# Performance work log

Hardware: AMD Instinct MI355X
Metric: run time of the kernel (lower is better)

The kernel has to match this reference:

```python
import jax, jax.numpy as jnp
import numpy as np

B, NQ, NV = 4, 16384, 16384
DIM, FRAMES = 64, 4
D = DIM * FRAMES            # embed_dims = 256
HEADS, POINTS, LEVELS = 8, 4, 1
HD = D // HEADS             # head_dim = 32
HL, WL = 128, 128           # single-level feature map, HL*WL == NV
EPS = 1e-6


def setup_inputs() -> dict:
    key = jax.random.key(0)
    ks = jax.random.split(key, 14)
    inp = {
        "query": jax.random.normal(ks[0], (B, NQ, D), jnp.float32),
        "feat": jax.random.normal(ks[1], (B, NV, D), jnp.float32),
        "reference_points": jax.random.uniform(ks[2], (B, NQ, LEVELS, 2), jnp.float32),
        "spatial_shapes": jnp.array([[HL, WL]], jnp.int32),
        "level_start_index": jnp.array([0], jnp.int32),
        # LayerNorm params
        "qn_scale": jnp.ones((D,), jnp.float32),
        "qn_bias": jnp.zeros((D,), jnp.float32),
        "fn_scale": jnp.ones((D,), jnp.float32),
        "fn_bias": jnp.zeros((D,), jnp.float32),
        # MSDeformAttn projections
        "W_value": jax.random.normal(ks[3], (D, D), jnp.float32) / np.sqrt(D),
        "b_value": jnp.zeros((D,), jnp.float32),
        "W_off": jax.random.normal(ks[4], (D, HEADS * LEVELS * POINTS * 2), jnp.float32) * 0.01,
        "b_off": jax.random.normal(ks[5], (HEADS * LEVELS * POINTS * 2,), jnp.float32) * 0.5,
        "W_attn": jax.random.normal(ks[6], (D, HEADS * LEVELS * POINTS), jnp.float32) * 0.02,
        "b_attn": jnp.zeros((HEADS * LEVELS * POINTS,), jnp.float32),
        "W_out": jax.random.normal(ks[7], (D, D), jnp.float32) / np.sqrt(D),
        "b_out": jnp.zeros((D,), jnp.float32),
        # gamma is a learned scale (init 0 in the module; randomized here so it contributes)
        "gamma": jax.random.normal(ks[8], (D,), jnp.float32) * 0.1,
    }
    return inp


def _layer_norm(x, scale, bias):
    mu = jnp.mean(x, axis=-1, keepdims=True)
    var = jnp.mean(jnp.square(x - mu), axis=-1, keepdims=True)
    return (x - mu) * jax.lax.rsqrt(var + EPS) * scale + bias


def _bilinear_gather(v, loc, Hl, Wl):
    # v:   [B, H, N, hd] flattened level values (row-major HxW)
    # loc: [B, H, NQ, P, 2] normalized sampling locations in [0,1]
    # grid_sample semantics: align_corners=False, zero padding
    x = loc[..., 0] * Wl - 0.5
    y = loc[..., 1] * Hl - 0.5
    x0 = jnp.floor(x); y0 = jnp.floor(y)
    x1 = x0 + 1.0;     y1 = y0 + 1.0
    wx1 = x - x0; wx0 = 1.0 - wx1
    wy1 = y - y0; wy0 = 1.0 - wy1
    out = 0.0
    for xi, yi, w in ((x0, y0, wx0 * wy0), (x1, y0, wx1 * wy0),
                      (x0, y1, wx0 * wy1), (x1, y1, wx1 * wy1)):
        inb = (xi >= 0) & (xi < Wl) & (yi >= 0) & (yi < Hl)
        idx = (jnp.clip(yi, 0, Hl - 1) * Wl + jnp.clip(xi, 0, Wl - 1)).astype(jnp.int32)
        Bc, Hc, NQc, Pc = idx.shape
        g = jnp.take_along_axis(v, idx.reshape(Bc, Hc, NQc * Pc)[..., None], axis=2)
        g = g.reshape(Bc, Hc, NQc, Pc, -1)          # [B, H, NQ, P, hd]
        out = out + g * (w * inb)[..., None]
    return out


def reference(query, feat, reference_points, spatial_shapes, level_start_index,
              qn_scale, qn_bias, fn_scale, fn_bias,
              W_value, b_value, W_off, b_off, W_attn, b_attn, W_out, b_out, gamma):
    Bq, nq, _ = query.shape
    q = _layer_norm(query, qn_scale, qn_bias)
    v = _layer_norm(feat, fn_scale, fn_bias)

    # value projection -> per-head values [B, H, NV, hd]
    value = (v @ W_value + b_value).reshape(Bq, -1, HEADS, HD).transpose(0, 2, 1, 3)

    # sampling offsets [B, NQ, H, L, P, 2] and attention weights (softmax over L*P)
    off = (q @ W_off + b_off).reshape(Bq, nq, HEADS, LEVELS, POINTS, 2)
    aw = jax.nn.softmax((q @ W_attn + b_attn).reshape(Bq, nq, HEADS, LEVELS * POINTS), axis=-1)
    aw = aw.reshape(Bq, nq, HEADS, LEVELS, POINTS)

    ss = np.asarray(spatial_shapes)          # static level geometry
    lsi = np.asarray(level_start_index)
    offset_norm = ss[:, ::-1].astype(np.float32)  # (W, H) per level
    # sampling locations [B, NQ, H, L, P, 2]
    loc = reference_points[:, :, None, :, None, :] + off / offset_norm[None, None, None, :, None, :]

    acc = jnp.zeros((Bq, HEADS, nq, HD), query.dtype)
    for l in range(LEVELS):
        Hl, Wl = int(ss[l, 0]), int(ss[l, 1])
        start = int(lsi[l])
        v_l = value[:, :, start:start + Hl * Wl]                # [B, H, Hl*Wl, hd]
        loc_l = loc[:, :, :, l].transpose(0, 2, 1, 3, 4)        # [B, H, NQ, P, 2]
        sampled = _bilinear_gather(v_l, loc_l, Hl, Wl)          # [B, H, NQ, P, hd]
        aw_l = aw[:, :, :, l].transpose(0, 2, 1, 3)             # [B, H, NQ, P]
        acc = acc + jnp.einsum('bhnpd,bhnp->bhnd', sampled, aw_l)

    out = acc.transpose(0, 2, 1, 3).reshape(Bq, nq, D) @ W_out + b_out
    return query + gamma * out
```

## Files before the change

kernel.cpp:

```cpp
#include <hip/hip_runtime.h>

#define NQ 16384
#define NV 16384
#define DMODEL 256
#define SAMPN (4 * 16384 * 8)
#define VPLANE 65536

typedef __bf16 bf16x8 __attribute__((ext_vector_type(8)));
typedef float f32x4 __attribute__((ext_vector_type(4)));

__device__ __forceinline__ unsigned short f2bf(float x) {
    union { float f; unsigned int u; } v; v.f = x;
    unsigned int r = v.u + 0x7fff + ((v.u >> 16) & 1);
    return (unsigned short)(r >> 16);
}
__device__ __forceinline__ float blo(unsigned int u) {
    union { unsigned int u; float f; } v; v.u = u << 16; return v.f;
}
__device__ __forceinline__ float bhi(unsigned int u) {
    union { unsigned int u; float f; } v; v.u = u & 0xFFFF0000u; return v.f;
}
__device__ __forceinline__ f32x4 mfma16(bf16x8 a, bf16x8 b, f32x4 c) {
    return __builtin_amdgcn_mfma_f32_16x16x32_bf16(a, b, c, 0, 0, 0);
}

__global__ __launch_bounds__(256) void k_prep(
    const float* __restrict__ Wv, const float* __restrict__ Woff,
    const float* __restrict__ Wattn, const float* __restrict__ Wout,
    const float* __restrict__ fns, const float* __restrict__ fnb,
    const float* __restrict__ qns, const float* __restrict__ qnb,
    const float* __restrict__ b_value, const float* __restrict__ b_off,
    const float* __restrict__ b_attn,
    unsigned short* __restrict__ WtV, unsigned short* __restrict__ WtC,
    unsigned short* __restrict__ WtO,
    float* __restrict__ csumV, float* __restrict__ preV,
    float* __restrict__ csumC, float* __restrict__ preC) {
    const int blk = blockIdx.x;
    if (blk < 608) {
        int t = blk * 256 + threadIdx.x;
        if (t < 65536) { int n = t >> 8, k = t & 255; WtV[t] = f2bf(fns[k] * Wv[k * 256 + n]); return; }
        t -= 65536;
        if (t < 65536) { int n = t >> 8, k = t & 255; WtO[t] = f2bf(Wout[k * 256 + n]); return; }
        t -= 65536;
        if (t < 24576) {
            int j = t >> 8, k = t & 255;
            float w = (j < 64) ? Woff[k * 64 + j] : Wattn[k * 32 + (j - 64)];
            WtC[j * 256 + k] = f2bf(qns[k] * w);
        }
        return;
    }
    if (blk < 612) {
        __shared__ float sCS[4][64], sPR[4][64];
        const int nl = threadIdx.x & 63;
        const int n = (blk - 608) * 64 + nl;
        const int kp = threadIdx.x >> 6;
        float cs = 0.f, pr = 0.f;
        for (int k = kp * 64; k < kp * 64 + 64; ++k) {
            float w = Wv[k * 256 + n];
            cs += fns[k] * w;
            pr += fnb[k] * w;
        }
        sCS[kp][nl] = cs; sPR[kp][nl] = pr;
        __syncthreads();
        if (threadIdx.x < 64) {
            int nn = (blk - 608) * 64 + threadIdx.x;
            csumV[nn] = sCS[0][threadIdx.x] + sCS[1][threadIdx.x] + sCS[2][threadIdx.x] + sCS[3][threadIdx.x];
            preV[nn] = sPR[0][threadIdx.x] + sPR[1][threadIdx.x] + sPR[2][threadIdx.x] + sPR[3][threadIdx.x]
                       + b_value[nn];
        }
        return;
    }
    {
        __shared__ float sCS[2][96], sPR[2][96];
        const int t = threadIdx.x;
        if (t < 192) {
            const int n = t % 96;
            const int kp = t / 96;
            float cs = 0.f, pr = 0.f;
            for (int k = kp * 128; k < kp * 128 + 128; ++k) {
                float w = (n < 64) ? Woff[k * 64 + n] : Wattn[k * 32 + (n - 64)];
                cs += qns[k] * w;
                pr += qnb[k] * w;
            }
            sCS[kp][n] = cs; sPR[kp][n] = pr;
        }
        __syncthreads();
        if (t < 96) {
            csumC[t] = sCS[0][t] + sCS[1][t];
            preC[t] = sPR[0][t] + sPR[1][t] + ((t < 64) ? b_off[t] : b_attn[t - 64]);
        }
        return;
    }
}

__global__ __launch_bounds__(256) void k_hist(
    const float* __restrict__ refpt, int* __restrict__ hist) {
    const int q = blockIdx.x * 256 + threadIdx.x;
    const int b = q >> 14;
    float rx = refpt[(size_t)q * 2 + 0], ry = refpt[(size_t)q * 2 + 1];
    int px = min(max((int)(rx * 128.f), 0), 127);
    int py = min(max((int)(ry * 128.f), 0), 127);
    int bucket = (b << 8) | ((py >> 3) << 4) | (px >> 3);
    atomicAdd(&hist[bucket], 1);
}

__global__ __launch_bounds__(256) void k_scan(
    const int* __restrict__ hist, int* __restrict__ base, int* __restrict__ cursor) {
    __shared__ int tmp[256];
    const int t = threadIdx.x;
    int4 h4 = ((const int4*)hist)[t];
    int tsum = h4.x + h4.y + h4.z + h4.w;
    tmp[t] = tsum;
    __syncthreads();
    for (int d = 1; d < 256; d <<= 1) {
        int v = (t >= d) ? tmp[t - d] : 0;
        __syncthreads();
        tmp[t] += v;
        __syncthreads();
    }
    int excl = tmp[t] - tsum;
    int4 b4;
    b4.x = excl; b4.y = excl + h4.x; b4.z = b4.y + h4.y; b4.w = b4.z + h4.z;
    ((int4*)base)[t] = b4;
    ((int4*)cursor)[t] = b4;
}

__global__ __launch_bounds__(256) void k_perm(
    const float* __restrict__ refpt, int* __restrict__ cursor, int* __restrict__ perm) {
    const int q = blockIdx.x * 256 + threadIdx.x;
    const int b = q >> 14;
    float rx = refpt[(size_t)q * 2 + 0], ry = refpt[(size_t)q * 2 + 1];
    int px = min(max((int)(rx * 128.f), 0), 127);
    int py = min(max((int)(ry * 128.f), 0), 127);
    int bucket = (b << 8) | ((py >> 3) << 4) | (px >> 3);
    int slot = atomicAdd(&cursor[bucket], 1);
    perm[slot] = q;
}

#define STAGE_LNSTATS64(srcptr)                                                       \
    {                                                                                 \
        const int t = threadIdx.x;                                                    \
        const float4* src4 = (const float4*)((srcptr) + (size_t)m0 * 256);            \
        _Pragma("unroll 8") for (int i = 0; i < 16; ++i) {                            \
            float4 x = src4[i * 256 + t];                                             \
            const int row = i * 4 + (t >> 6);                                         \
            uint2 pk;                                                                 \
            pk.x = (unsigned)f2bf(x.x) | ((unsigned)f2bf(x.y) << 16);                 \
            pk.y = (unsigned)f2bf(x.z) | ((unsigned)f2bf(x.w) << 16);                 \
            *(uint2*)&A[row * 264 + (t & 63) * 4] = pk;                               \
        }                                                                             \
    }                                                                                 \
    __syncthreads();                                                                  \
    {                                                                                 \
        const int t = threadIdx.x;                                                    \
        const int r = t >> 2, h = t & 3;                                              \
        float s = 0.f, sq = 0.f;                                                      \
        _Pragma("unroll") for (int j = 0; j < 8; ++j) {                               \
            uint4 u = *(const uint4*)&A[r * 264 + h * 64 + j * 8];                    \
            float v0 = blo(u.x), v1 = bhi(u.x), v2 = blo(u.y), v3 = bhi(u.y);         \
            float v4 = blo(u.z), v5 = bhi(u.z), v6 = blo(u.w), v7 = bhi(u.w);         \
            s += v0 + v1 + v2 + v3 + v4 + v5 + v6 + v7;                               \
            sq += v0 * v0 + v1 * v1 + v2 * v2 + v3 * v3 +                             \
                  v4 * v4 + v5 * v5 + v6 * v6 + v7 * v7;                              \
        }                                                                             \
        s += __shfl_xor(s, 1);  sq += __shfl_xor(sq, 1);                              \
        s += __shfl_xor(s, 2);  sq += __shfl_xor(sq, 2);                              \
        if (h == 0) {                                                                 \
            float mu = s * 0.00390625f;                                               \
            muL[r] = mu;                                                              \
            rsL[r] = rsqrtf(sq * 0.00390625f - mu * mu + 1e-6f);                      \
        }                                                                             \
    }

#define MFMA_STEP4(bf, kk)                                                            \
    _Pragma("unroll") for (int m = 0; m < 4; ++m) {                                   \
        bf16x8 a = *(const bf16x8*)&A[(m * 16 + lrow) * 264 + (kk) * 32 + lk];        \
        _Pragma("unroll") for (int i = 0; i < 4; ++i)                                 \
            acc[i][m] = mfma16(bf[i], a, acc[i][m]);                                  \
    }

__global__ __launch_bounds__(256, 4) void k_mlp(
    const float* __restrict__ feat, const float* __restrict__ csumV,
    const float* __restrict__ preV, const unsigned short* __restrict__ WtV,
    unsigned short* __restrict__ value,
    const float* __restrict__ query, const float* __restrict__ refpt,
    const float* __restrict__ csumC, const float* __restrict__ preC,
    const unsigned short* __restrict__ WtC, float4* __restrict__ samples) {
    __shared__ unsigned short A[64 * 264];
    __shared__ float muL[64], rsL[64];
    const int blk = blockIdx.x;
    const int m0 = (blk >> 1) * 64;
    const int lane = threadIdx.x & 63;
    const int w = threadIdx.x >> 6;

    if ((blk & 1) == 0) {
        STAGE_LNSTATS64(feat)
        const int lrow = lane & 15, lk = (lane >> 4) * 8;
        f32x4 acc[4][4];
#pragma unroll
        for (int i = 0; i < 4; ++i)
#pragma unroll
            for (int m = 0; m < 4; ++m) acc[i][m] = (f32x4){0.f, 0.f, 0.f, 0.f};
#define LOADB_V(dst, kk)                                                              \
    _Pragma("unroll") for (int i = 0; i < 4; ++i) dst[i] =                            \
        *(const bf16x8*)(WtV + (size_t)((w * 4 + i) * 16 + lrow) * 256 + (kk) * 32 + lk);
        {
            bf16x8 b0[4], b1[4];
            LOADB_V(b0, 0)
#pragma unroll
            for (int k2 = 0; k2 < 4; ++k2) {
                LOADB_V(b1, k2 * 2 + 1)
                MFMA_STEP4(b0, k2 * 2)
                if (k2 < 3) { LOADB_V(b0, k2 * 2 + 2) }
                MFMA_STEP4(b1, k2 * 2 + 1)
            }
        }
        __syncthreads();
        const int g = lane >> 4;
#pragma unroll
        for (int i = 0; i < 4; ++i) {
            const int col0 = (w * 4 + i) * 16 + g * 4;
            float4 cs = *(const float4*)(csumV + col0);
            float4 pr = *(const float4*)(preV + col0);
#pragma unroll
            for (int m = 0; m < 4; ++m) {
                const int rl = m * 16 + (lane & 15);
                float mu = muL[rl], rs = rsL[rl];
                uint2 r;
                r.x = (unsigned)f2bf(rs * (acc[i][m][0] - mu * cs.x) + pr.x) |
                      ((unsigned)f2bf(rs * (acc[i][m][1] - mu * cs.y) + pr.y) << 16);
                r.y = (unsigned)f2bf(rs * (acc[i][m][2] - mu * cs.z) + pr.z) |
                      ((unsigned)f2bf(rs * (acc[i][m][3] - mu * cs.w) + pr.w) << 16);
                *(uint2*)&A[rl * 264 + col0] = r;
            }
        }
        __syncthreads();
        {
            const int pix = threadIdx.x >> 2;
            const int chunk = threadIdx.x & 3;
#pragma unroll
            for (int h = 0; h < 8; ++h) {
                *(uint4*)(value + ((size_t)h * VPLANE + (m0 + pix)) * 32 + chunk * 8) =
                    *(uint4*)&A[pix * 264 + h * 32 + chunk * 8];
            }
        }
    } else {
        float* DlA = (float*)A;
        const int lrow = lane & 15, g = lane >> 4, lk = g * 8;
        const float4* qrow = (const float4*)(query + (size_t)(m0 + w * 16 + lrow) * 256) + g * 2;
        f32x4 acc[6];
#pragma unroll
        for (int i = 0; i < 6; ++i) acc[i] = (f32x4){0.f, 0.f, 0.f, 0.f};
        float s = 0.f, sq = 0.f;
#pragma unroll
        for (int kk = 0; kk < 8; ++kk) {
            float4 xa = qrow[kk * 8];
            float4 xb = qrow[kk * 8 + 1];
            s  += xa.x + xa.y + xa.z + xa.w + xb.x + xb.y + xb.z + xb.w;
            sq += xa.x * xa.x + xa.y * xa.y + xa.z * xa.z + xa.w * xa.w +
                  xb.x * xb.x + xb.y * xb.y + xb.z * xb.z + xb.w * xb.w;
            union { bf16x8 v; unsigned short u[8]; } af;
            af.u[0] = f2bf(xa.x); af.u[1] = f2bf(xa.y); af.u[2] = f2bf(xa.z); af.u[3] = f2bf(xa.w);
            af.u[4] = f2bf(xb.x); af.u[5] = f2bf(xb.y); af.u[6] = f2bf(xb.z); af.u[7] = f2bf(xb.w);
            bf16x8 b[6];
#pragma unroll
            for (int i = 0; i < 6; ++i)
                b[i] = *(const bf16x8*)(WtC + (size_t)(i * 16 + lrow) * 256 + kk * 32 + lk);
#pragma unroll
            for (int i = 0; i < 6; ++i) acc[i] = mfma16(b[i], af.v, acc[i]);
        }
        s += __shfl_xor(s, 16); sq += __shfl_xor(sq, 16);
        s += __shfl_xor(s, 32); sq += __shfl_xor(sq, 32);
        if (lane < 16) {
            float mu = s * 0.00390625f;
            muL[w * 16 + lane] = mu;
            rsL[w * 16 + lane] = rsqrtf(sq * 0.00390625f - mu * mu + 1e-6f);
        }
        float* Dl = DlA + w * 1600;
#pragma unroll
        for (int i = 0; i < 6; ++i) {
            *(float4*)&Dl[lrow * 100 + i * 16 + g * 4] =
                make_float4(acc[i][0], acc[i][1], acc[i][2], acc[i][3]);
        }
        __syncthreads();
#pragma unroll
        for (int it = 0; it < 2; ++it) {
            int idx = it * 64 + lane;
            int rl = idx >> 3;
            int h = idx & 7;
            int row = m0 + w * 16 + rl;
            float mu = muL[w * 16 + rl], rs = rsL[w * 16 + rl];
            float rx = refpt[(size_t)row * 2 + 0] * 128.f - 0.5f;
            float ry = refpt[(size_t)row * 2 + 1] * 128.f - 0.5f;
            float l0 = rs * (Dl[rl * 100 + 64 + h * 4 + 0] - mu * csumC[64 + h * 4 + 0]) + preC[64 + h * 4 + 0];
            float l1 = rs * (Dl[rl * 100 + 64 + h * 4 + 1] - mu * csumC[64 + h * 4 + 1]) + preC[64 + h * 4 + 1];
            float l2 = rs * (Dl[rl * 100 + 64 + h * 4 + 2] - mu * csumC[64 + h * 4 + 2]) + preC[64 + h * 4 + 2];
            float l3 = rs * (Dl[rl * 100 + 64 + h * 4 + 3] - mu * csumC[64 + h * 4 + 3]) + preC[64 + h * 4 + 3];
            float mx = fmaxf(fmaxf(l0, l1), fmaxf(l2, l3));
            float e0 = __expf(l0 - mx), e1 = __expf(l1 - mx);
            float e2 = __expf(l2 - mx), e3 = __expf(l3 - mx);
            float inv = 1.f / (e0 + e1 + e2 + e3);
            float ww[4] = {e0 * inv, e1 * inv, e2 * inv, e3 * inv};
            size_t trow = (size_t)row * 8 + h;
#pragma unroll
            for (int p = 0; p < 4; ++p) {
                float ox = rs * (Dl[rl * 100 + h * 8 + p * 2 + 0] - mu * csumC[h * 8 + p * 2 + 0]) + preC[h * 8 + p * 2 + 0];
                float oy = rs * (Dl[rl * 100 + h * 8 + p * 2 + 1] - mu * csumC[h * 8 + p * 2 + 1]) + preC[h * 8 + p * 2 + 1];
                samples[(size_t)p * SAMPN + trow] = make_float4(rx + ox, ry + oy, ww[p], 0.f);
            }
        }
    }
}

__global__ __launch_bounds__(256, 4) void k_gatherout(
    const unsigned short* __restrict__ value, const float4* __restrict__ samples,
    const int* __restrict__ perm,
    const unsigned short* __restrict__ WtO, const float* __restrict__ b_out,
    const float* __restrict__ gamma, const float* __restrict__ query,
    float* __restrict__ out) {
    __shared__ unsigned short A[64 * 264];
    __shared__ int permL[64];
    const int m0 = blockIdx.x * 64;
    if (threadIdx.x < 64) permL[threadIdx.x] = perm[m0 + threadIdx.x];
    __syncthreads();
    {
        const int t = threadIdx.x;
        const int h = (t >> 2) & 7;
        const int sub = t & 3;
#pragma unroll
        for (int k = 0; k < 8; ++k) {
            const int rl = k * 8 + (t >> 5);
            const int qp = permL[rl];
            const int bq = qp >> 14;
            const unsigned short* vb =
                value + ((size_t)h * VPLANE + ((size_t)bq << 14)) * 32 + sub * 8;
            const size_t trow = (size_t)qp * 8 + h;
            float a0 = 0.f, a1 = 0.f, a2 = 0.f, a3 = 0.f;
            float a4 = 0.f, a5 = 0.f, a6 = 0.f, a7 = 0.f;
#pragma unroll
            for (int p = 0; p < 4; ++p) {
                float4 s = samples[(size_t)p * SAMPN + trow];
                float xf = floorf(s.x), yf = floorf(s.y);
                float fx = s.x - xf, fy = s.y - yf;
                int x0 = (int)xf, y0 = (int)yf;
                int x1 = x0 + 1, y1 = y0 + 1;
                float wgt = s.z;
                bool bx0 = (unsigned)x0 < 128u, bx1 = (unsigned)x1 < 128u;
                bool by0 = (unsigned)y0 < 128u, by1 = (unsigned)y1 < 128u;
                float wt[4];
                wt[0] = (bx0 && by0) ? (1.f - fx) * (1.f - fy) * wgt : 0.f;
                wt[1] = (bx1 && by0) ? fx * (1.f - fy) * wgt : 0.f;
                wt[2] = (bx0 && by1) ? (1.f - fx) * fy * wgt : 0.f;
                wt[3] = (bx1 && by1) ? fx * fy * wgt : 0.f;
                int xc0 = min(max(x0, 0), 127), xc1 = min(max(x1, 0), 127);
                int yc0 = min(max(y0, 0), 127), yc1 = min(max(y1, 0), 127);
                int pix[4];
                pix[0] = yc0 * 128 + xc0; pix[1] = yc0 * 128 + xc1;
                pix[2] = yc1 * 128 + xc0; pix[3] = yc1 * 128 + xc1;
#pragma unroll
                for (int tp = 0; tp < 4; ++tp) {
                    uint4 u = *(const uint4*)(vb + (size_t)pix[tp] * 32);
                    float wq = wt[tp];
                    a0 = fmaf(wq, blo(u.x), a0); a1 = fmaf(wq, bhi(u.x), a1);
                    a2 = fmaf(wq, blo(u.y), a2); a3 = fmaf(wq, bhi(u.y), a3);
                    a4 = fmaf(wq, blo(u.z), a4); a5 = fmaf(wq, bhi(u.z), a5);
                    a6 = fmaf(wq, blo(u.w), a6); a7 = fmaf(wq, bhi(u.w), a7);
                }
            }
            uint4 r;
            r.x = (unsigned)f2bf(a0) | ((unsigned)f2bf(a1) << 16);
            r.y = (unsigned)f2bf(a2) | ((unsigned)f2bf(a3) << 16);
            r.z = (unsigned)f2bf(a4) | ((unsigned)f2bf(a5) << 16);
            r.w = (unsigned)f2bf(a6) | ((unsigned)f2bf(a7) << 16);
            *(uint4*)&A[rl * 264 + h * 32 + sub * 8] = r;
        }
    }
    __syncthreads();
    const int lane = threadIdx.x & 63;
    const int w = threadIdx.x >> 6;
    const int lrow = lane & 15, lk = (lane >> 4) * 8;
    f32x4 acc[4][4];
#pragma unroll
    for (int i = 0; i < 4; ++i)
#pragma unroll
        for (int m = 0; m < 4; ++m) acc[i][m] = (f32x4){0.f, 0.f, 0.f, 0.f};
#define LOADB_O(dst, kk)                                                              \
    _Pragma("unroll") for (int i = 0; i < 4; ++i) dst[i] =                            \
        *(const bf16x8*)(WtO + (size_t)((w * 4 + i) * 16 + lrow) * 256 + (kk) * 32 + lk);
    {
        bf16x8 b0[4], b1[4];
        LOADB_O(b0, 0)
#pragma unroll
        for (int k2 = 0; k2 < 4; ++k2) {
            LOADB_O(b1, k2 * 2 + 1)
            MFMA_STEP4(b0, k2 * 2)
            if (k2 < 3) { LOADB_O(b0, k2 * 2 + 2) }
            MFMA_STEP4(b1, k2 * 2 + 1)
        }
    }
    const int g = lane >> 4;
    float4 bo[4], gm[4];
#pragma unroll
    for (int i = 0; i < 4; ++i) {
        bo[i] = *(const float4*)(b_out + (w * 4 + i) * 16 + g * 4);
        gm[i] = *(const float4*)(gamma + (w * 4 + i) * 16 + g * 4);
    }
#pragma unroll
    for (int m = 0; m < 4; ++m) {
        const size_t row = (size_t)permL[m * 16 + (lane & 15)];
#pragma unroll
        for (int i = 0; i < 4; ++i) {
            const int col0 = (w * 4 + i) * 16 + g * 4;
            float4 q = *(const float4*)(query + row * 256 + col0);
            float4 o;
            o.x = q.x + gm[i].x * (acc[i][m][0] + bo[i].x);
            o.y = q.y + gm[i].y * (acc[i][m][1] + bo[i].y);
            o.z = q.z + gm[i].z * (acc[i][m][2] + bo[i].z);
            o.w = q.w + gm[i].w * (acc[i][m][3] + bo[i].w);
            *(float4*)(out + row * 256 + col0) = o;
        }
    }
}

extern "C" void kernel_launch(void* const* d_in, const int* in_sizes, int n_in,
                              void* d_out, int out_size, void* d_ws, size_t ws_size,
                              hipStream_t stream) {
    const float* query    = (const float*)d_in[0];
    const float* feat     = (const float*)d_in[1];
    const float* refpt    = (const float*)d_in[2];
    const float* qn_scale = (const float*)d_in[5];
    const float* qn_bias  = (const float*)d_in[6];
    const float* fn_scale = (const float*)d_in[7];
    const float* fn_bias  = (const float*)d_in[8];
    const float* W_value  = (const float*)d_in[9];
    const float* b_value  = (const float*)d_in[10];
    const float* W_off    = (const float*)d_in[11];
    const float* b_off    = (const float*)d_in[12];
    const float* W_attn   = (const float*)d_in[13];
    const float* b_attn   = (const float*)d_in[14];
    const float* W_out    = (const float*)d_in[15];
    const float* b_out    = (const float*)d_in[16];
    const float* gamma    = (const float*)d_in[17];
    float* out = (float*)d_out;

    char* ws = (char*)d_ws;
    unsigned short* WtV   = (unsigned short*)(ws);
    unsigned short* WtO   = (unsigned short*)(ws + 131072);
    unsigned short* WtC   = (unsigned short*)(ws + 262144);
    float* csumV = (float*)(ws + 311296);
    float* preV  = (float*)(ws + 312320);
    float* csumC = (float*)(ws + 313344);
    float* preC  = (float*)(ws + 313856);
    int* hist    = (int*)(ws + 314368);
    int* basep   = (int*)(ws + 318464);
    int* cursor  = (int*)(ws + 322560);
    int* perm    = (int*)(ws + 326656);
    unsigned short* value = (unsigned short*)(ws + 655360);
    float4* samples       = (float4*)(ws + 655360 + 33554432);

    hipMemsetAsync(ws + 314368, 0, 12288, stream);
    hipLaunchKernelGGL(k_prep, dim3(613), dim3(256), 0, stream,
                       W_value, W_off, W_attn, W_out,
                       fn_scale, fn_bias, qn_scale, qn_bias,
                       b_value, b_off, b_attn,
                       WtV, WtC, WtO, csumV, preV, csumC, preC);
    hipLaunchKernelGGL(k_hist, dim3(256), dim3(256), 0, stream, refpt, hist);
    hipLaunchKernelGGL(k_scan, dim3(1), dim3(256), 0, stream, hist, basep, cursor);
    hipLaunchKernelGGL(k_perm, dim3(256), dim3(256), 0, stream, refpt, cursor, perm);
    hipLaunchKernelGGL(k_mlp, dim3(2048), dim3(256), 0, stream,
                       feat, csumV, preV, WtV, value,
                       query, refpt, csumC, preC, WtC, samples);
    hipLaunchKernelGGL(k_gatherout, dim3(1024), dim3(256), 0, stream,
                       value, samples, perm, WtO, b_out, gamma, query, out);
}
```

Baseline: 177.3 us.

## Split fused gather+output-projection kernel into separate gather and GEMM kernels

The fused gather/output-projection kernel is split in two. A standalone gather kernel runs one sample row per thread over 8192 blocks in permuted order and writes bf16 accumulators to a workspace buffer in natural query order. A separate MFMA kernel then stages those rows into LDS and applies the output projection, writing rows in natural order. This gives the latency-bound gather higher occupancy, since it no longer carries the GEMM's LDS and register footprint. The cost is an extra 32 MB bf16 round trip through global memory and one more kernel launch.

```diff
diff --git a/kernel.cpp b/kernel.cpp
--- a/kernel.cpp
+++ b/kernel.cpp
@@ -172,6 +172,17 @@
         }                                                                             \
     }
 
+#define STAGE_A64(srcbuf)                                                             \
+    {                                                                                 \
+        const int c = threadIdx.x & 31;                                               \
+        const int rt = threadIdx.x >> 5;                                              \
+        _Pragma("unroll") for (int i = 0; i < 8; ++i) {                               \
+            const int r = rt + i * 8;                                                 \
+            *(uint4*)&A[r * 264 + c * 8] =                                            \
+                *(const uint4*)((srcbuf) + (size_t)(m0 + r) * 256 + c * 8);           \
+        }                                                                             \
+    }
+
 #define MFMA_STEP4(bf, kk)                                                            \
     _Pragma("unroll") for (int m = 0; m < 4; ++m) {                                   \
         bf16x8 a = *(const bf16x8*)&A[(m * 16 + lrow) * 264 + (kk) * 32 + lk];        \
@@ -312,69 +323,66 @@
     }
 }
 
-__global__ __launch_bounds__(256, 4) void k_gatherout(
+__global__ __launch_bounds__(256) void k_gather(
     const unsigned short* __restrict__ value, const float4* __restrict__ samples,
-    const int* __restrict__ perm,
-    const unsigned short* __restrict__ WtO, const float* __restrict__ b_out,
-    const float* __restrict__ gamma, const float* __restrict__ query,
-    float* __restrict__ out) {
+    const int* __restrict__ perm, unsigned short* __restrict__ accb) {
+    const int tid = blockIdx.x * 256 + threadIdx.x;
+    const int sub = tid & 3;
+    const int t = tid >> 2;
+    const int h = t & 7;
+    const int slot = t >> 3;
+    const int q = perm[slot];
+    const int b = q >> 14;
+    const unsigned short* vb =
+        value + ((size_t)h * VPLANE + ((size_t)b << 14)) * 32 + sub * 8;
+    const size_t trow = (size_t)q * 8 + h;
+    float a0 = 0.f, a1 = 0.f, a2 = 0.f, a3 = 0.f;
+    float a4 = 0.f, a5 = 0.f, a6 = 0.f, a7 = 0.f;
+#pragma unroll
+    for (int p = 0; p < 4; ++p) {
+        float4 s = samples[(size_t)p * SAMPN + trow];
+        float xf = floorf(s.x), yf = floorf(s.y);
+        float fx = s.x - xf, fy = s.y - yf;
+        int x0 = (int)xf, y0 = (int)yf;
+        int x1 = x0 + 1, y1 = y0 + 1;
+        float wgt = s.z;
+        bool bx0 = (unsigned)x0 < 128u, bx1 = (unsigned)x1 < 128u;
+        bool by0 = (unsigned)y0 < 128u, by1 = (unsigned)y1 < 128u;
+        float wt[4];
+        wt[0] = (bx0 && by0) ? (1.f - fx) * (1.f - fy) * wgt : 0.f;
+        wt[1] = (bx1 && by0) ? fx * (1.f - fy) * wgt : 0.f;
+        wt[2] = (bx0 && by1) ? (1.f - fx) * fy * wgt : 0.f;
+        wt[3] = (bx1 && by1) ? fx * fy * wgt : 0.f;
+        int xc0 = min(max(x0, 0), 127), xc1 = min(max(x1, 0), 127);
+        int yc0 = min(max(y0, 0), 127), yc1 = min(max(y1, 0), 127);
+        int pix[4];
+        pix[0] = yc0 * 128 + xc0; pix[1] = yc0 * 128 + xc1;
+        pix[2] = yc1 * 128 + xc0; pix[3] = yc1 * 128 + xc1;
+#pragma unroll
+        for (int tp = 0; tp < 4; ++tp) {
+            uint4 u = *(const uint4*)(vb + (size_t)pix[tp] * 32);
+            float wq = wt[tp];
+            a0 = fmaf(wq, blo(u.x), a0); a1 = fmaf(wq, bhi(u.x), a1);
+            a2 = fmaf(wq, blo(u.y), a2); a3 = fmaf(wq, bhi(u.y), a3);
+            a4 = fmaf(wq, blo(u.z), a4); a5 = fmaf(wq, bhi(u.z), a5);
+            a6 = fmaf(wq, blo(u.w), a6); a7 = fmaf(wq, bhi(u.w), a7);
+        }
+    }
+    uint4 r;
+    r.x = (unsigned)f2bf(a0) | ((unsigned)f2bf(a1) << 16);
+    r.y = (unsigned)f2bf(a2) | ((unsigned)f2bf(a3) << 16);
+    r.z = (unsigned)f2bf(a4) | ((unsigned)f2bf(a5) << 16);
+    r.w = (unsigned)f2bf(a6) | ((unsigned)f2bf(a7) << 16);
+    *(uint4*)(accb + (size_t)q * 256 + h * 32 + sub * 8) = r;
+}
+
+__global__ __launch_bounds__(256, 4) void k_out(
+    const unsigned short* __restrict__ accb, const unsigned short* __restrict__ WtO,
+    const float* __restrict__ b_out, const float* __restrict__ gamma,
+    const float* __restrict__ query, float* __restrict__ out) {
     __shared__ unsigned short A[64 * 264];
-    __shared__ int permL[64];
     const int m0 = blockIdx.x * 64;
-    if (threadIdx.x < 64) permL[threadIdx.x] = perm[m0 + threadIdx.x];
-    __syncthreads();
-    {
-        const int t = threadIdx.x;
-        const int h = (t >> 2) & 7;
-        const int sub = t & 3;
-#pragma unroll
-        for (int k = 0; k < 8; ++k) {
-            const int rl = k * 8 + (t >> 5);
-            const int qp = permL[rl];
-            const int bq = qp >> 14;
-            const unsigned short* vb =
-                value + ((size_t)h * VPLANE + ((size_t)bq << 14)) * 32 + sub * 8;
-            const size_t trow = (size_t)qp * 8 + h;
-            float a0 = 0.f, a1 = 0.f, a2 = 0.f, a3 = 0.f;
-            float a4 = 0.f, a5 = 0.f, a6 = 0.f, a7 = 0.f;
-#pragma unroll
-            for (int p = 0; p < 4; ++p) {
-                float4 s = samples[(size_t)p * SAMPN + trow];
-                float xf = floorf(s.x), yf = floorf(s.y);
-                float fx = s.x - xf, fy = s.y - yf;
-                int x0 = (int)xf, y0 = (int)yf;
-                int x1 = x0 + 1, y1 = y0 + 1;
-                float wgt = s.z;
-                bool bx0 = (unsigned)x0 < 128u, bx1 = (unsigned)x1 < 128u;
-                bool by0 = (unsigned)y0 < 128u, by1 = (unsigned)y1 < 128u;
-                float wt[4];
-                wt[0] = (bx0 && by0) ? (1.f - fx) * (1.f - fy) * wgt : 0.f;
-                wt[1] = (bx1 && by0) ? fx * (1.f - fy) * wgt : 0.f;
-                wt[2] = (bx0 && by1) ? (1.f - fx) * fy * wgt : 0.f;
-                wt[3] = (bx1 && by1) ? fx * fy * wgt : 0.f;
-                int xc0 = min(max(x0, 0), 127), xc1 = min(max(x1, 0), 127);
-                int yc0 = min(max(y0, 0), 127), yc1 = min(max(y1, 0), 127);
-                int pix[4];
-                pix[0] = yc0 * 128 + xc0; pix[1] = yc0 * 128 + xc1;
-                pix[2] = yc1 * 128 + xc0; pix[3] = yc1 * 128 + xc1;
-#pragma unroll
-                for (int tp = 0; tp < 4; ++tp) {
-                    uint4 u = *(const uint4*)(vb + (size_t)pix[tp] * 32);
-                    float wq = wt[tp];
-                    a0 = fmaf(wq, blo(u.x), a0); a1 = fmaf(wq, bhi(u.x), a1);
-                    a2 = fmaf(wq, blo(u.y), a2); a3 = fmaf(wq, bhi(u.y), a3);
-                    a4 = fmaf(wq, blo(u.z), a4); a5 = fmaf(wq, bhi(u.z), a5);
-                    a6 = fmaf(wq, blo(u.w), a6); a7 = fmaf(wq, bhi(u.w), a7);
-                }
-            }
-            uint4 r;
-            r.x = (unsigned)f2bf(a0) | ((unsigned)f2bf(a1) << 16);
-            r.y = (unsigned)f2bf(a2) | ((unsigned)f2bf(a3) << 16);
-            r.z = (unsigned)f2bf(a4) | ((unsigned)f2bf(a5) << 16);
-            r.w = (unsigned)f2bf(a6) | ((unsigned)f2bf(a7) << 16);
-            *(uint4*)&A[rl * 264 + h * 32 + sub * 8] = r;
-        }
-    }
+    STAGE_A64(accb)
     __syncthreads();
     const int lane = threadIdx.x & 63;
     const int w = threadIdx.x >> 6;
@@ -407,7 +415,7 @@
     }
 #pragma unroll
     for (int m = 0; m < 4; ++m) {
-        const size_t row = (size_t)permL[m * 16 + (lane & 15)];
+        const size_t row = (size_t)(m0 + m * 16 + (lane & 15));
 #pragma unroll
         for (int i = 0; i < 4; ++i) {
             const int col0 = (w * 4 + i) * 16 + g * 4;
@@ -457,6 +465,7 @@
     int* perm    = (int*)(ws + 326656);
     unsigned short* value = (unsigned short*)(ws + 655360);
     float4* samples       = (float4*)(ws + 655360 + 33554432);
+    unsigned short* accb  = (unsigned short*)(ws + 655360 + 2 * 33554432);
 
     hipMemsetAsync(ws + 314368, 0, 12288, stream);
     hipLaunchKernelGGL(k_prep, dim3(613), dim3(256), 0, stream,
@@ -470,6 +479,8 @@
     hipLaunchKernelGGL(k_mlp, dim3(2048), dim3(256), 0, stream,
                        feat, csumV, preV, WtV, value,
                        query, refpt, csumC, preC, WtC, samples);
-    hipLaunchKernelGGL(k_gatherout, dim3(1024), dim3(256), 0, stream,
-                       value, samples, perm, WtO, b_out, gamma, query, out);
-}
+    hipLaunchKernelGGL(k_gather, dim3(8192), dim3(256), 0, stream,
+                       value, samples, perm, accb);
+    hipLaunchKernelGGL(k_out, dim3(1024), dim3(256), 0, stream,
+                       accb, WtO, b_out, gamma, query, out);
+}
```

New measurement: 195.6 us. 10.4% more time.
